# Performance work log

Measured on AMD Instinct MI355X. Metric: run time of the kernel, lower is better.

Reference implementation:

```python
import jax, jax.numpy as jnp
import numpy as np

LEAK = 0.9
BASE_THRESH = 1.0
BN_EPS = 1e-5

@jax.custom_vjp
def spike_fn(x):
    return (x >= 0).astype(x.dtype)

def _spike_fwd(x):
    return (x >= 0).astype(x.dtype), x

def _spike_bwd(x, g):
    return (g / (1.0 + 5.0 * jnp.abs(x)) ** 2,)

spike_fn.defvjp(_spike_fwd, _spike_bwd)


def setup_inputs() -> dict:
    key = jax.random.key(0)
    ks = jax.random.split(key, 8)
    B, T, C, H, NC, DT = 256, 2048, 64, 64, 4, 50
    kin_spikes_seq = jax.random.normal(ks[0], (B, T, C), dtype=jnp.float32)
    tda_features = jax.random.normal(ks[1], (B, DT), dtype=jnp.float32)
    # spatial_conv1x1: Linear(64 -> 64, bias=False); weight [out, in]
    W_spatial = jax.random.normal(ks[2], (H, C), dtype=jnp.float32) / np.sqrt(C)
    bn_gamma = jnp.ones((H,), dtype=jnp.float32)
    bn_beta = jnp.zeros((H,), dtype=jnp.float32)
    # class_conv1x1: Linear(64 -> 4, bias=False)
    W_class = jax.random.normal(ks[3], (NC, H), dtype=jnp.float32) / np.sqrt(H)
    lateral = jnp.eye(NC, dtype=jnp.float32) * 0.8 - 0.1
    # tda_to_thresh: Linear(50 -> 4)
    W_tda = jax.random.normal(ks[4], (NC, DT), dtype=jnp.float32) / np.sqrt(DT)
    b_tda = jnp.zeros((NC,), dtype=jnp.float32)
    return {
        "kin_spikes_seq": kin_spikes_seq,
        "tda_features": tda_features,
        "W_spatial": W_spatial,
        "bn_gamma": bn_gamma,
        "bn_beta": bn_beta,
        "W_class": W_class,
        "lateral": lateral,
        "W_tda": W_tda,
        "b_tda": b_tda,
    }


def reference(kin_spikes_seq, tda_features, W_spatial, bn_gamma, bn_beta,
              W_class, lateral, W_tda, b_tda):
    # [B, T, C] @ [C, H] -> [B, T, H]
    x_proj = jnp.einsum("btc,hc->bth", kin_spikes_seq, W_spatial)
    # BatchNorm1d in training mode: per-channel stats over (B, T)
    mean = jnp.mean(x_proj, axis=(0, 1))
    var = jnp.var(x_proj, axis=(0, 1))
    x_proj = (x_proj - mean) * jax.lax.rsqrt(var + BN_EPS) * bn_gamma + bn_beta

    tda_mod = jax.nn.sigmoid(tda_features @ W_tda.T + b_tda) * 0.5  # [B, 4]
    dynamic_thresh = BASE_THRESH + tda_mod

    B = kin_spikes_seq.shape[0]
    H, NC = W_class.shape[1], W_class.shape[0]
    mem1 = jnp.zeros((B, H), dtype=x_proj.dtype)
    mem2 = jnp.zeros((B, NC), dtype=x_proj.dtype)
    spike_sum = jnp.zeros((B, NC), dtype=x_proj.dtype)

    def step(carry, xt):
        mem1, mem2, ssum = carry
        mem1 = LEAK * mem1 + xt
        spk1 = spike_fn(mem1 - BASE_THRESH)
        mem1 = mem1 * (1.0 - spk1)
        cur2 = (spk1 @ W_class.T) @ lateral  # [B, 4]
        mem2 = LEAK * mem2 + cur2
        spk2 = spike_fn(mem2 - dynamic_thresh)
        mem2 = mem2 * (1.0 - spk2)
        return (mem1, mem2, ssum + spk2), None

    xs = jnp.swapaxes(x_proj, 0, 1)  # [T, B, H]
    (mem1, mem2, spike_sum), _ = jax.lax.scan(step, (mem1, mem2, spike_sum), xs)
    return spike_sum
```

## Files before the change

kernel.cpp:

```cpp
#include <hip/hip_runtime.h>
#include <cstdint>
#include <cstddef>

#define BB 256
#define TB 2048
#define NROWS (BB*TB)
#define R1 256
#define NBLK_K1 (NROWS/R1)
#define NBLK1 4096

typedef float f32x4 __attribute__((ext_vector_type(4)));

#define OFF_X      0ull
#define SZ_X       ((size_t)NROWS*64*4)
#define OFF_PART   (OFF_X + SZ_X)
#define SZ_PART    ((size_t)128*NBLK1*4)
#define OFF_STAT   (OFF_PART + SZ_PART)
#define SZ_STAT    (128*8)
#define OFF_PARAM  (OFF_STAT + SZ_STAT)
#define SZ_PARAM   ((size_t)(64+64+1024)*4)
#define OFF_MASK   ((OFF_PARAM + SZ_PARAM + 255ull) & ~255ull)
#define SZ_MASK    ((size_t)NROWS*8)
#define OFF_CUR2   (OFF_MASK + SZ_MASK)
#define SZ_CUR2    ((size_t)NROWS*4*4)

__global__ __launch_bounds__(256, 2) void k1_gemm(const float* __restrict__ kin,
                                                  const float* __restrict__ Wsp,
                                                  float* __restrict__ xproj,
                                                  float* __restrict__ partials) {
  __shared__ float4 As[R1 * 16];
  __shared__ float4 Ws4[64 * 16];
  const int tid = threadIdx.x;
  const size_t r0 = (size_t)blockIdx.x * R1;

  const f32x4* kin4 = (const f32x4*)(kin + r0 * 64);
  #pragma unroll
  for (int k = 0; k < 16; ++k) {
    int idx = k * 256 + tid;
    int r = idx >> 4, cc = idx & 15;
    f32x4 v = __builtin_nontemporal_load(&kin4[idx]);
    As[r * 16 + (cc ^ ((r >> 3) & 7))] = make_float4(v.x, v.y, v.z, v.w);
  }
  const float4* W4 = (const float4*)Wsp;
  #pragma unroll
  for (int k = 0; k < 4; ++k) {
    int idx = k * 256 + tid;
    int h = idx >> 4, cc = idx & 15;
    Ws4[h * 16 + (cc ^ ((h >> 3) & 7))] = W4[idx];
  }
  __syncthreads();

  const int ty = tid >> 3;
  const int tx = tid & 7;
  float acc[8][8];
  #pragma unroll
  for (int i = 0; i < 8; ++i)
    #pragma unroll
    for (int j = 0; j < 8; ++j) acc[i][j] = 0.f;

  #pragma unroll 1
  for (int cc = 0; cc < 16; ++cc) {
    float4 av[8], wv[8];
    #pragma unroll
    for (int i = 0; i < 8; ++i)
      av[i] = As[(8 * ty + i) * 16 + (cc ^ (ty & 7))];
    #pragma unroll
    for (int j = 0; j < 8; ++j)
      wv[j] = Ws4[(8 * tx + j) * 16 + (cc ^ tx)];
    #pragma unroll
    for (int i = 0; i < 8; ++i)
      #pragma unroll
      for (int j = 0; j < 8; ++j) {
        acc[i][j] = fmaf(av[i].x, wv[j].x, acc[i][j]);
        acc[i][j] = fmaf(av[i].y, wv[j].y, acc[i][j]);
        acc[i][j] = fmaf(av[i].z, wv[j].z, acc[i][j]);
        acc[i][j] = fmaf(av[i].w, wv[j].w, acc[i][j]);
      }
  }

  #pragma unroll
  for (int i = 0; i < 8; ++i) {
    const size_t row = r0 + 8 * ty + i;
    *(float4*)(xproj + row * 64 + 8 * tx) =
        make_float4(acc[i][0], acc[i][1], acc[i][2], acc[i][3]);
    *(float4*)(xproj + row * 64 + 8 * tx + 4) =
        make_float4(acc[i][4], acc[i][5], acc[i][6], acc[i][7]);
  }

  __syncthreads();
  float* Sm = (float*)As;
  float* Sq = Sm + 64 * 33;
  #pragma unroll
  for (int j = 0; j < 8; ++j) {
    const int col = 8 * tx + j;
    float s = 0.f, q = 0.f;
    #pragma unroll
    for (int i = 0; i < 8; ++i) {
      s += acc[i][j];
      q += acc[i][j] * acc[i][j];
    }
    Sm[col * 33 + ty] = s;
    Sq[col * 33 + ty] = q;
  }
  __syncthreads();
  if (tid < 64) {
    float s0 = 0.f, q0 = 0.f, s1 = 0.f, q1 = 0.f;
    #pragma unroll
    for (int g = 0; g < 16; ++g)  { s0 += Sm[tid * 33 + g]; q0 += Sq[tid * 33 + g]; }
    #pragma unroll
    for (int g = 16; g < 32; ++g) { s1 += Sm[tid * 33 + g]; q1 += Sq[tid * 33 + g]; }
    const size_t p0 = 2 * (size_t)blockIdx.x;
    partials[(size_t)tid * NBLK1 + p0]            = s0;
    partials[(size_t)tid * NBLK1 + p0 + 1]        = s1;
    partials[(size_t)(64 + tid) * NBLK1 + p0]     = q0;
    partials[(size_t)(64 + tid) * NBLK1 + p0 + 1] = q1;
  }
}

__global__ __launch_bounds__(256) void k2a_reduce(const float* __restrict__ partials,
                                                  double* __restrict__ statd) {
  __shared__ double sd[256];
  const int idx = blockIdx.x;
  double acc = 0.0;
  for (int k = threadIdx.x; k < NBLK1; k += 256)
    acc += (double)partials[(size_t)idx * NBLK1 + k];
  sd[threadIdx.x] = acc;
  __syncthreads();
  for (int s = 128; s > 0; s >>= 1) {
    if (threadIdx.x < s) sd[threadIdx.x] += sd[threadIdx.x + s];
    __syncthreads();
  }
  if (threadIdx.x == 0) statd[idx] = sd[0];
}

__global__ __launch_bounds__(256) void k2b_final(const double* __restrict__ statd,
                                                 const float* __restrict__ gamma,
                                                 const float* __restrict__ beta,
                                                 const float* __restrict__ tda,
                                                 const float* __restrict__ Wtda,
                                                 const float* __restrict__ btda,
                                                 float* __restrict__ param) {
  const int tid = threadIdx.x, blk = blockIdx.x;
  if (blk == 4) {
    if (tid < 64) {
      double mean = statd[tid] / (double)NROWS;
      double ex2  = statd[64 + tid] / (double)NROWS;
      double var  = ex2 - mean * mean;
      double sc   = (double)gamma[tid] / sqrt(var + 1e-5);
      param[tid]      = (float)sc;
      param[64 + tid] = (float)((double)beta[tid] - mean * sc);
    }
    return;
  }
  const int g = blk * 256 + tid;
  const int b = g >> 2, j = g & 3;
  double acc = (double)btda[j];
  for (int k = 0; k < 50; ++k)
    acc += (double)tda[b * 50 + k] * (double)Wtda[j * 50 + k];
  double sig = 1.0 / (1.0 + exp(-acc));
  param[128 + g] = (float)(1.0 + 0.5 * sig);
}

#define K3_LOAD(BUF, TBASE)                         \
  { _Pragma("unroll") for (int i_ = 0; i_ < 64; ++i_) \
      BUF[i_] = xr[(size_t)((TBASE) + i_) * 64]; }

#define K3_CHUNK(CUR, NXT0, TBASE)                                   \
  { unsigned long long keep = 0;                                     \
    _Pragma("unroll") for (int i_ = 0; i_ < 64; ++i_) {              \
      bool sp = (mem >= 1.0f);                                       \
      unsigned long long mb = __ballot(sp);                          \
      if (h == i_) keep = mb;                                        \
      float xrn = (i_ < 63) ? CUR[(i_ + 1) & 63] : (NXT0);           \
      float xn = fmaf(xrn, sc, sh);                                  \
      mem = sp ? xn : fmaf(mem, 0.9f, xn);                           \
    }                                                                \
    masksB[(size_t)b * TB + (TBASE) + h] = keep; }

__global__ __launch_bounds__(64) void k3_scan1(const float* __restrict__ xproj,
                                               const float* __restrict__ param,
                                               unsigned long long* __restrict__ masksB) {
  const int b = blockIdx.x, h = threadIdx.x;
  const float sc = param[h], sh = param[64 + h];
  const float* xr = xproj + (size_t)b * TB * 64 + h;
  float xa[64], xb[64];

  K3_LOAD(xa, 0)
  float mem = fmaf(xa[0], sc, sh);

  #pragma unroll 1
  for (int t0 = 0; t0 < TB; t0 += 128) {
    K3_LOAD(xb, t0 + 64)
    K3_CHUNK(xa, xb[0], t0)
    if (t0 + 128 < TB) { K3_LOAD(xa, t0 + 128) }
    K3_CHUNK(xb, xa[0], t0 + 64)
  }
}

__global__ __launch_bounds__(256) void k4_cur2(const unsigned long long* __restrict__ masksB,
                                               const float* __restrict__ Wc,
                                               const float* __restrict__ lat,
                                               float* __restrict__ cur2T) {
  __shared__ float WcL[256];
  __shared__ float latL[16];
  const int tid = threadIdx.x, b = blockIdx.x;
  WcL[tid] = Wc[tid];
  if (tid < 16) latL[tid] = lat[tid];
  __syncthreads();

  #pragma unroll 1
  for (int c = 0; c < 8; ++c) {
    const int t = c * 256 + tid;
    const unsigned long long m = masksB[(size_t)b * TB + t];
    const unsigned lo = (unsigned)m, hi = (unsigned)(m >> 32);
    float v0 = 0.f, v1 = 0.f, v2 = 0.f, v3 = 0.f;
    #pragma unroll
    for (int hh = 0; hh < 32; ++hh) {
      const float bit = (float)((lo >> hh) & 1u);
      v0 = fmaf(bit, WcL[hh],       v0);
      v1 = fmaf(bit, WcL[64 + hh],  v1);
      v2 = fmaf(bit, WcL[128 + hh], v2);
      v3 = fmaf(bit, WcL[192 + hh], v3);
    }
    #pragma unroll
    for (int hh = 32; hh < 64; ++hh) {
      const float bit = (float)((hi >> (hh - 32)) & 1u);
      v0 = fmaf(bit, WcL[hh],       v0);
      v1 = fmaf(bit, WcL[64 + hh],  v1);
      v2 = fmaf(bit, WcL[128 + hh], v2);
      v3 = fmaf(bit, WcL[192 + hh], v3);
    }
    float o0, o1, o2, o3;
    { float cx = v0 * latL[0];  cx = fmaf(v1, latL[4],  cx); cx = fmaf(v2, latL[8],  cx); cx = fmaf(v3, latL[12], cx); o0 = cx; }
    { float cx = v0 * latL[1];  cx = fmaf(v1, latL[5],  cx); cx = fmaf(v2, latL[9],  cx); cx = fmaf(v3, latL[13], cx); o1 = cx; }
    { float cx = v0 * latL[2];  cx = fmaf(v1, latL[6],  cx); cx = fmaf(v2, latL[10], cx); cx = fmaf(v3, latL[14], cx); o2 = cx; }
    { float cx = v0 * latL[3];  cx = fmaf(v1, latL[7],  cx); cx = fmaf(v2, latL[11], cx); cx = fmaf(v3, latL[15], cx); o3 = cx; }
    cur2T[(size_t)(b * 4 + 0) * TB + t] = o0;
    cur2T[(size_t)(b * 4 + 1) * TB + t] = o1;
    cur2T[(size_t)(b * 4 + 2) * TB + t] = o2;
    cur2T[(size_t)(b * 4 + 3) * TB + t] = o3;
  }
}

#define K5_LOAD(BUF, TBASE)                                              \
  { _Pragma("unroll") for (int k_ = 0; k_ < 16; ++k_) {                  \
      float4 v = cr[((TBASE) >> 2) + k_];                                \
      BUF[4 * k_] = v.x; BUF[4 * k_ + 1] = v.y;                          \
      BUF[4 * k_ + 2] = v.z; BUF[4 * k_ + 3] = v.w; } }

#define K5_CHUNK(CUR, NXT0)                                   \
  { _Pragma("unroll") for (int i_ = 0; i_ < 64; ++i_) {       \
      bool sp = (mem >= th);                                  \
      cnt += sp ? 1u : 0u;                                    \
      float xn = (i_ < 63) ? CUR[(i_ + 1) & 63] : (NXT0);     \
      mem = sp ? xn : fmaf(mem, 0.9f, xn);                    \
    } }

__global__ __launch_bounds__(64) void k5_scan2(const float* __restrict__ cur2T,
                                               const float* __restrict__ param,
                                               float* __restrict__ out) {
  const int b = blockIdx.x;
  const int j4 = threadIdx.x & 3;
  const int g = b * 4 + j4;
  const float th = param[128 + g];
  const float4* cr = (const float4*)(cur2T + (size_t)g * TB);
  float ca[64], cb[64];

  K5_LOAD(ca, 0)
  float mem = ca[0];
  unsigned cnt = 0;

  #pragma unroll 1
  for (int t0 = 0; t0 < TB; t0 += 128) {
    K5_LOAD(cb, t0 + 64)
    K5_CHUNK(ca, cb[0])
    if (t0 + 128 < TB) { K5_LOAD(ca, t0 + 128) }
    K5_CHUNK(cb, ca[0])
  }
  if (threadIdx.x < 4) out[g] = (float)cnt;
}

extern "C" void kernel_launch(void* const* d_in, const int* in_sizes, int n_in,
                              void* d_out, int out_size, void* d_ws, size_t ws_size,
                              hipStream_t stream) {
  const float* kin   = (const float*)d_in[0];
  const float* tda   = (const float*)d_in[1];
  const float* Wsp   = (const float*)d_in[2];
  const float* gamma = (const float*)d_in[3];
  const float* beta  = (const float*)d_in[4];
  const float* Wc    = (const float*)d_in[5];
  const float* lat   = (const float*)d_in[6];
  const float* Wtda  = (const float*)d_in[7];
  const float* btda  = (const float*)d_in[8];

  char* ws = (char*)d_ws;
  float*  xproj    = (float*)(ws + OFF_X);
  float*  partials = (float*)(ws + OFF_PART);
  double* statd    = (double*)(ws + OFF_STAT);
  float*  param    = (float*)(ws + OFF_PARAM);
  unsigned long long* masksB = (unsigned long long*)(ws + OFF_MASK);
  float*  cur2T    = (float*)(ws + OFF_CUR2);
  float*  out      = (float*)d_out;

  k1_gemm  <<<dim3(NBLK_K1), dim3(256), 0, stream>>>(kin, Wsp, xproj, partials);
  k2a_reduce<<<dim3(128),  dim3(256), 0, stream>>>(partials, statd);
  k2b_final<<<dim3(5),     dim3(256), 0, stream>>>(statd, gamma, beta, tda, Wtda, btda, param);
  k3_scan1 <<<dim3(BB),    dim3(64),  0, stream>>>(xproj, param, masksB);
  k4_cur2  <<<dim3(BB),    dim3(256), 0, stream>>>(masksB, Wc, lat, cur2T);
  k5_scan2 <<<dim3(BB),    dim3(64),  0, stream>>>(cur2T, param, out);
}
```

Baseline: 163.7 us.

## Fuse cur2 and second scan via LDS; register-stream A in GEMM with packed FMA

The cur2 projection kernel and the second-layer scan are merged into one kernel. The per-timestep cur2 values now pass through shared memory instead of a global round trip, which also removes one launch. The GEMM kernel now reads its input rows straight into registers with double buffering instead of staging them in LDS. It uses a pair-interleaved, swizzled weight layout so the inner loop can issue packed two-wide FMAs. Risks include higher register pressure in the GEMM, and the fused kernel's scan uses only 64 of its 256 threads while holding about 32KB of LDS.

```diff
diff --git a/kernel.cpp b/kernel.cpp
--- a/kernel.cpp
+++ b/kernel.cpp
@@ -10,6 +10,7 @@
 #define NBLK1 4096
 
 typedef float f32x4 __attribute__((ext_vector_type(4)));
+typedef float f32x2 __attribute__((ext_vector_type(2)));
 
 #define OFF_X      0ull
 #define SZ_X       ((size_t)NROWS*64*4)
@@ -21,83 +22,90 @@
 #define SZ_PARAM   ((size_t)(64+64+1024)*4)
 #define OFF_MASK   ((OFF_PARAM + SZ_PARAM + 255ull) & ~255ull)
 #define SZ_MASK    ((size_t)NROWS*8)
-#define OFF_CUR2   (OFF_MASK + SZ_MASK)
-#define SZ_CUR2    ((size_t)NROWS*4*4)
 
 __global__ __launch_bounds__(256, 2) void k1_gemm(const float* __restrict__ kin,
                                                   const float* __restrict__ Wsp,
                                                   float* __restrict__ xproj,
                                                   float* __restrict__ partials) {
-  __shared__ float4 As[R1 * 16];
-  __shared__ float4 Ws4[64 * 16];
+  __shared__ f32x4 Wp[32 * 32];
+  __shared__ float Sm[64 * 33];
+  __shared__ float Sq[64 * 33];
   const int tid = threadIdx.x;
+  const int ty = tid >> 3;
+  const int tx = tid & 7;
   const size_t r0 = (size_t)blockIdx.x * R1;
 
-  const f32x4* kin4 = (const f32x4*)(kin + r0 * 64);
-  #pragma unroll
-  for (int k = 0; k < 16; ++k) {
-    int idx = k * 256 + tid;
-    int r = idx >> 4, cc = idx & 15;
-    f32x4 v = __builtin_nontemporal_load(&kin4[idx]);
-    As[r * 16 + (cc ^ ((r >> 3) & 7))] = make_float4(v.x, v.y, v.z, v.w);
-  }
-  const float4* W4 = (const float4*)Wsp;
+  const float* abase = kin + (r0 + 8 * (size_t)ty) * 64;
+  f32x4 av[2][8];
+  #pragma unroll
+  for (int i = 0; i < 8; ++i)
+    av[0][i] = __builtin_nontemporal_load((const f32x4*)(abase + i * 64 + 0));
+  #pragma unroll
+  for (int i = 0; i < 8; ++i)
+    av[1][i] = __builtin_nontemporal_load((const f32x4*)(abase + i * 64 + 4));
+
   #pragma unroll
   for (int k = 0; k < 4; ++k) {
     int idx = k * 256 + tid;
-    int h = idx >> 4, cc = idx & 15;
-    Ws4[h * 16 + (cc ^ ((h >> 3) & 7))] = W4[idx];
-  }
-  __syncthreads();
-
-  const int ty = tid >> 3;
-  const int tx = tid & 7;
-  float acc[8][8];
+    int p = idx >> 5, q = idx & 31;
+    float2 w0 = *(const float2*)(Wsp + (2 * p) * 64 + 2 * q);
+    float2 w1 = *(const float2*)(Wsp + (2 * p + 1) * 64 + 2 * q);
+    Wp[p * 32 + (q ^ ((p >> 2) & 7))] = (f32x4){w0.x, w1.x, w0.y, w1.y};
+  }
+  __syncthreads();
+
+  f32x2 acc2[8][4];
   #pragma unroll
   for (int i = 0; i < 8; ++i)
     #pragma unroll
-    for (int j = 0; j < 8; ++j) acc[i][j] = 0.f;
-
-  #pragma unroll 1
+    for (int jp = 0; jp < 4; ++jp) acc2[i][jp] = (f32x2){0.f, 0.f};
+
+  #pragma unroll
   for (int cc = 0; cc < 16; ++cc) {
-    float4 av[8], wv[8];
-    #pragma unroll
-    for (int i = 0; i < 8; ++i)
-      av[i] = As[(8 * ty + i) * 16 + (cc ^ (ty & 7))];
-    #pragma unroll
-    for (int j = 0; j < 8; ++j)
-      wv[j] = Ws4[(8 * tx + j) * 16 + (cc ^ tx)];
-    #pragma unroll
-    for (int i = 0; i < 8; ++i)
+    const int buf = cc & 1;
+    f32x4 q0[4], q1[4];
+    #pragma unroll
+    for (int jp = 0; jp < 4; ++jp) {
+      const int p = 4 * tx + jp;
+      q0[jp] = Wp[p * 32 + ((2 * cc)     ^ tx)];
+      q1[jp] = Wp[p * 32 + ((2 * cc + 1) ^ tx)];
+    }
+    #pragma unroll
+    for (int i = 0; i < 8; ++i) {
+      f32x4 a = av[buf][i];
       #pragma unroll
-      for (int j = 0; j < 8; ++j) {
-        acc[i][j] = fmaf(av[i].x, wv[j].x, acc[i][j]);
-        acc[i][j] = fmaf(av[i].y, wv[j].y, acc[i][j]);
-        acc[i][j] = fmaf(av[i].z, wv[j].z, acc[i][j]);
-        acc[i][j] = fmaf(av[i].w, wv[j].w, acc[i][j]);
+      for (int jp = 0; jp < 4; ++jp) {
+        acc2[i][jp] = __builtin_elementwise_fma((f32x2){a.x, a.x}, q0[jp].xy, acc2[i][jp]);
+        acc2[i][jp] = __builtin_elementwise_fma((f32x2){a.y, a.y}, q0[jp].zw, acc2[i][jp]);
+        acc2[i][jp] = __builtin_elementwise_fma((f32x2){a.z, a.z}, q1[jp].xy, acc2[i][jp]);
+        acc2[i][jp] = __builtin_elementwise_fma((f32x2){a.w, a.w}, q1[jp].zw, acc2[i][jp]);
       }
+    }
+    if (cc < 14) {
+      #pragma unroll
+      for (int i = 0; i < 8; ++i)
+        av[buf][i] = __builtin_nontemporal_load((const f32x4*)(abase + i * 64 + (cc + 2) * 4));
+    }
   }
 
   #pragma unroll
   for (int i = 0; i < 8; ++i) {
     const size_t row = r0 + 8 * ty + i;
-    *(float4*)(xproj + row * 64 + 8 * tx) =
-        make_float4(acc[i][0], acc[i][1], acc[i][2], acc[i][3]);
-    *(float4*)(xproj + row * 64 + 8 * tx + 4) =
-        make_float4(acc[i][4], acc[i][5], acc[i][6], acc[i][7]);
-  }
-
-  __syncthreads();
-  float* Sm = (float*)As;
-  float* Sq = Sm + 64 * 33;
+    f32x4 lo = {acc2[i][0].x, acc2[i][0].y, acc2[i][1].x, acc2[i][1].y};
+    f32x4 hi = {acc2[i][2].x, acc2[i][2].y, acc2[i][3].x, acc2[i][3].y};
+    *(f32x4*)(xproj + row * 64 + 8 * tx)     = lo;
+    *(f32x4*)(xproj + row * 64 + 8 * tx + 4) = hi;
+  }
+
   #pragma unroll
   for (int j = 0; j < 8; ++j) {
     const int col = 8 * tx + j;
     float s = 0.f, q = 0.f;
     #pragma unroll
     for (int i = 0; i < 8; ++i) {
-      s += acc[i][j];
-      q += acc[i][j] * acc[i][j];
+      float v = (j & 1) ? acc2[i][j >> 1].y : acc2[i][j >> 1].x;
+      s += v;
+      q += v * v;
     }
     Sm[col * 33 + ty] = s;
     Sq[col * 33 + ty] = q;
@@ -197,12 +205,28 @@
   }
 }
 
-__global__ __launch_bounds__(256) void k4_cur2(const unsigned long long* __restrict__ masksB,
-                                               const float* __restrict__ Wc,
-                                               const float* __restrict__ lat,
-                                               float* __restrict__ cur2T) {
+#define K45_LOAD(BUF, TBASE)                                             \
+  { _Pragma("unroll") for (int k_ = 0; k_ < 16; ++k_) {                  \
+      f32x4 v = *(const f32x4*)(cr + (TBASE) + 4 * k_);                  \
+      BUF[4 * k_] = v.x; BUF[4 * k_ + 1] = v.y;                          \
+      BUF[4 * k_ + 2] = v.z; BUF[4 * k_ + 3] = v.w; } }
+
+#define K45_CHUNK(CUR, NXT0)                                  \
+  { _Pragma("unroll") for (int i_ = 0; i_ < 64; ++i_) {       \
+      bool sp = (mem >= th);                                  \
+      cnt += sp ? 1u : 0u;                                    \
+      float xn = (i_ < 63) ? CUR[(i_ + 1) & 63] : (NXT0);     \
+      mem = sp ? xn : fmaf(mem, 0.9f, xn);                    \
+    } }
+
+__global__ __launch_bounds__(256) void k45_cur2scan(const unsigned long long* __restrict__ masksB,
+                                                    const float* __restrict__ Wc,
+                                                    const float* __restrict__ lat,
+                                                    const float* __restrict__ param,
+                                                    float* __restrict__ out) {
   __shared__ float WcL[256];
   __shared__ float latL[16];
+  __shared__ float lbuf[4][TB + 4];
   const int tid = threadIdx.x, b = blockIdx.x;
   WcL[tid] = Wc[tid];
   if (tid < 16) latL[tid] = lat[tid];
@@ -230,54 +254,31 @@
       v2 = fmaf(bit, WcL[128 + hh], v2);
       v3 = fmaf(bit, WcL[192 + hh], v3);
     }
-    float o0, o1, o2, o3;
-    { float cx = v0 * latL[0];  cx = fmaf(v1, latL[4],  cx); cx = fmaf(v2, latL[8],  cx); cx = fmaf(v3, latL[12], cx); o0 = cx; }
-    { float cx = v0 * latL[1];  cx = fmaf(v1, latL[5],  cx); cx = fmaf(v2, latL[9],  cx); cx = fmaf(v3, latL[13], cx); o1 = cx; }
-    { float cx = v0 * latL[2];  cx = fmaf(v1, latL[6],  cx); cx = fmaf(v2, latL[10], cx); cx = fmaf(v3, latL[14], cx); o2 = cx; }
-    { float cx = v0 * latL[3];  cx = fmaf(v1, latL[7],  cx); cx = fmaf(v2, latL[11], cx); cx = fmaf(v3, latL[15], cx); o3 = cx; }
-    cur2T[(size_t)(b * 4 + 0) * TB + t] = o0;
-    cur2T[(size_t)(b * 4 + 1) * TB + t] = o1;
-    cur2T[(size_t)(b * 4 + 2) * TB + t] = o2;
-    cur2T[(size_t)(b * 4 + 3) * TB + t] = o3;
-  }
-}
-
-#define K5_LOAD(BUF, TBASE)                                              \
-  { _Pragma("unroll") for (int k_ = 0; k_ < 16; ++k_) {                  \
-      float4 v = cr[((TBASE) >> 2) + k_];                                \
-      BUF[4 * k_] = v.x; BUF[4 * k_ + 1] = v.y;                          \
-      BUF[4 * k_ + 2] = v.z; BUF[4 * k_ + 3] = v.w; } }
-
-#define K5_CHUNK(CUR, NXT0)                                   \
-  { _Pragma("unroll") for (int i_ = 0; i_ < 64; ++i_) {       \
-      bool sp = (mem >= th);                                  \
-      cnt += sp ? 1u : 0u;                                    \
-      float xn = (i_ < 63) ? CUR[(i_ + 1) & 63] : (NXT0);     \
-      mem = sp ? xn : fmaf(mem, 0.9f, xn);                    \
-    } }
-
-__global__ __launch_bounds__(64) void k5_scan2(const float* __restrict__ cur2T,
-                                               const float* __restrict__ param,
-                                               float* __restrict__ out) {
-  const int b = blockIdx.x;
-  const int j4 = threadIdx.x & 3;
-  const int g = b * 4 + j4;
-  const float th = param[128 + g];
-  const float4* cr = (const float4*)(cur2T + (size_t)g * TB);
+    { float cx = v0 * latL[0];  cx = fmaf(v1, latL[4],  cx); cx = fmaf(v2, latL[8],  cx); cx = fmaf(v3, latL[12], cx); lbuf[0][t] = cx; }
+    { float cx = v0 * latL[1];  cx = fmaf(v1, latL[5],  cx); cx = fmaf(v2, latL[9],  cx); cx = fmaf(v3, latL[13], cx); lbuf[1][t] = cx; }
+    { float cx = v0 * latL[2];  cx = fmaf(v1, latL[6],  cx); cx = fmaf(v2, latL[10], cx); cx = fmaf(v3, latL[14], cx); lbuf[2][t] = cx; }
+    { float cx = v0 * latL[3];  cx = fmaf(v1, latL[7],  cx); cx = fmaf(v2, latL[11], cx); cx = fmaf(v3, latL[15], cx); lbuf[3][t] = cx; }
+  }
+  __syncthreads();
+  if (tid >= 64) return;
+
+  const int j4 = tid & 3;
+  const float th = param[128 + b * 4 + j4];
+  const float* cr = lbuf[j4];
   float ca[64], cb[64];
 
-  K5_LOAD(ca, 0)
+  K45_LOAD(ca, 0)
   float mem = ca[0];
   unsigned cnt = 0;
 
   #pragma unroll 1
   for (int t0 = 0; t0 < TB; t0 += 128) {
-    K5_LOAD(cb, t0 + 64)
-    K5_CHUNK(ca, cb[0])
-    if (t0 + 128 < TB) { K5_LOAD(ca, t0 + 128) }
-    K5_CHUNK(cb, ca[0])
-  }
-  if (threadIdx.x < 4) out[g] = (float)cnt;
+    K45_LOAD(cb, t0 + 64)
+    K45_CHUNK(ca, cb[0])
+    if (t0 + 128 < TB) { K45_LOAD(ca, t0 + 128) }
+    K45_CHUNK(cb, ca[0])
+  }
+  if (tid < 4) out[b * 4 + j4] = (float)cnt;
 }
 
 extern "C" void kernel_launch(void* const* d_in, const int* in_sizes, int n_in,
@@ -299,13 +300,11 @@
   double* statd    = (double*)(ws + OFF_STAT);
   float*  param    = (float*)(ws + OFF_PARAM);
   unsigned long long* masksB = (unsigned long long*)(ws + OFF_MASK);
-  float*  cur2T    = (float*)(ws + OFF_CUR2);
   float*  out      = (float*)d_out;
 
   k1_gemm  <<<dim3(NBLK_K1), dim3(256), 0, stream>>>(kin, Wsp, xproj, partials);
   k2a_reduce<<<dim3(128),  dim3(256), 0, stream>>>(partials, statd);
   k2b_final<<<dim3(5),     dim3(256), 0, stream>>>(statd, gamma, beta, tda, Wtda, btda, param);
   k3_scan1 <<<dim3(BB),    dim3(64),  0, stream>>>(xproj, param, masksB);
-  k4_cur2  <<<dim3(BB),    dim3(256), 0, stream>>>(masksB, Wc, lat, cur2T);
-  k5_scan2 <<<dim3(BB),    dim3(64),  0, stream>>>(cur2T, param, out);
-}
+  k45_cur2scan<<<dim3(BB), dim3(256), 0, stream>>>(masksB, Wc, lat, param, out);
+}
```

Result: slower. 254.8 us (+55.7%).
